# Performance work log

Measured on AMD Instinct MI355X. Metric: run time of the kernel, lower is better.

Reference implementation:

```python
import jax, jax.numpy as jnp
import numpy as np

N = 2_097_152          # n_transitions = n_envs * buffer_size
GAMMA = 0.99
GAE_LAMBDA = 0.95
CLIP_EPS = 0.2
NORM_ADVANTAGES = True


def setup_inputs() -> dict:
    key = jax.random.key(0)
    ks = jax.random.split(key, 7)
    f = lambda k: jax.random.normal(k, (N, 1), dtype=jnp.float32)
    return {
        "rewards": f(ks[0]),
        "values": f(ks[1]),
        "next_values": f(ks[2]),
        "log_probs": -jnp.abs(f(ks[3])),       # log-probs are <= 0
        "old_log_probs": -jnp.abs(f(ks[4])),
        "terminated": jax.random.randint(ks[5], (N, 1), 0, 2).astype(bool),
        "truncated": jax.random.randint(ks[6], (N, 1), 0, 2).astype(bool),
    }


def reference(rewards, values, next_values, log_probs, old_log_probs,
              terminated, truncated):
    dtype = rewards.dtype
    dones = jnp.logical_or(terminated, truncated)
    not_term = 1.0 - terminated.astype(dtype)          # [N,1]
    not_done = 1.0 - dones.astype(dtype)               # [N,1]

    # TD residuals: delta_n = r_n + gamma * (1 - terminated_n) * V(s'_n) - V(s_n)
    deltas = rewards + GAMMA * not_term * next_values - values   # [N,1]

    # Reverse GAE recurrence (the torch Python for-loop, fused into one scan):
    # adv_n = (1 - done_n) * gamma * lambda * adv_{n+1} + delta_n
    coef = not_done[:, 0] * (GAMMA * GAE_LAMBDA)       # [N]

    def step(adv, cd):
        c, d = cd
        adv = c * adv + d
        return adv, adv

    _, advantages = jax.lax.scan(step, jnp.zeros((), dtype),
                                 (coef, deltas[:, 0]), reverse=True)
    advantages = advantages[:, None]                   # [N,1]

    lambda_returns = advantages + values               # [N,1]

    if NORM_ADVANTAGES:
        # torch .std() is the unbiased (ddof=1) estimator
        adv_n = (advantages - advantages.mean()) / (
            jnp.std(advantages, ddof=1) + 1e-9)
    else:
        adv_n = advantages

    # PPO clipped surrogate, per-sample (the .mean() is a trivial reduction)
    ratio = jnp.exp(log_probs - old_log_probs)
    clamped = jnp.clip(ratio, 1.0 - CLIP_EPS, 1.0 + CLIP_EPS)
    per_sample_actor_loss = -jnp.minimum(ratio * adv_n, clamped * adv_n)

    # [N,3]: normalized advantages, lambda returns, per-sample clipped objective
    return jnp.concatenate([adv_n, lambda_returns, per_sample_actor_loss], axis=1)
```

## Files before the change

### kernel.cpp

```cpp
#include <hip/hip_runtime.h>
#include <stdint.h>

static constexpr int BLOCK = 256;
static constexpr int ITEMS = 16;
static constexpr int CHUNK = BLOCK * ITEMS;
static constexpr int MAXNB = 512;

#define GAMMA_F 0.99f
static __device__ __forceinline__ float gl_const() { return (float)(0.99 * 0.95); }

__device__ __forceinline__ int detect_mode(const void* term, int n_elems, int* flg) {
    int t = threadIdx.x;
    if (t == 0) { flg[0] = 0; flg[1] = 0; }
    __syncthreads();
    if (t < 256) {
        const unsigned char* p = (const unsigned char*)term;
        int i0 = 4 * t;
        if (i0 + 3 < n_elems) {
            unsigned b1 = p[i0 + 1], b2 = p[i0 + 2], b3 = p[i0 + 3];
            if (b1) atomicOr(&flg[0], 1);
            if (b2 | b3) atomicOr(&flg[1], 1);
        }
    }
    __syncthreads();
    return flg[0] ? 1 : (flg[1] ? 2 : 0);
}

__device__ __forceinline__ int load_bool1(const void* p, long i, int mode) {
    if (mode == 1) return ((const unsigned char*)p)[i] != 0;
    if (mode == 0) return ((const int*)p)[i] != 0;
    return ((const float*)p)[i] != 0.0f;
}

__device__ __forceinline__ void load_bool16(const void* p, long base, int mode, int* f) {
    if (mode == 1) {
        uint4 q = *(const uint4*)((const unsigned char*)p + base);
        unsigned w[4] = {q.x, q.y, q.z, q.w};
#pragma unroll
        for (int j = 0; j < 16; ++j) f[j] = (int)((w[j >> 2] >> ((j & 3) * 8)) & 0xffu);
    } else if (mode == 0) {
        const int4* q = (const int4*)((const int*)p + base);
#pragma unroll
        for (int k = 0; k < 4; ++k) {
            int4 v = q[k];
            f[4*k] = v.x; f[4*k+1] = v.y; f[4*k+2] = v.z; f[4*k+3] = v.w;
        }
    } else {
        const float4* q = (const float4*)((const float*)p + base);
#pragma unroll
        for (int k = 0; k < 4; ++k) {
            float4 v = q[k];
            f[4*k] = v.x != 0.f; f[4*k+1] = v.y != 0.f; f[4*k+2] = v.z != 0.f; f[4*k+3] = v.w != 0.f;
        }
    }
}

__device__ __forceinline__ void compute_cd(
    const float* __restrict__ rewards, const float* __restrict__ values,
    const float* __restrict__ next_values, const void* __restrict__ term,
    const void* __restrict__ trunc, int mode, long base, int n,
    float* c, float* d, float* v)
{
    const float GL = gl_const();
    if (base + ITEMS <= n) {
        float r[ITEMS], nv[ITEMS];
        const float4* r4 = (const float4*)(rewards + base);
        const float4* v4 = (const float4*)(values + base);
        const float4* n4 = (const float4*)(next_values + base);
#pragma unroll
        for (int k = 0; k < 4; ++k) {
            float4 a = r4[k]; r[4*k]=a.x; r[4*k+1]=a.y; r[4*k+2]=a.z; r[4*k+3]=a.w;
            float4 b = v4[k]; v[4*k]=b.x; v[4*k+1]=b.y; v[4*k+2]=b.z; v[4*k+3]=b.w;
            float4 q = n4[k]; nv[4*k]=q.x; nv[4*k+1]=q.y; nv[4*k+2]=q.z; nv[4*k+3]=q.w;
        }
        int tm[ITEMS], tr[ITEMS];
        load_bool16(term,  base, mode, tm);
        load_bool16(trunc, base, mode, tr);
#pragma unroll
        for (int j = 0; j < ITEMS; ++j) {
            float nt = tm[j] ? 0.f : 1.f;
            float nd = (tm[j] | tr[j]) ? 0.f : 1.f;
            d[j] = r[j] + GAMMA_F * nt * nv[j] - v[j];
            c[j] = nd * GL;
        }
    } else {
#pragma unroll
        for (int j = 0; j < ITEMS; ++j) {
            long i = base + j;
            if (i < (long)n) {
                int tm = load_bool1(term, i, mode);
                int tr = load_bool1(trunc, i, mode);
                float nt = tm ? 0.f : 1.f;
                float nd = (tm | tr) ? 0.f : 1.f;
                v[j] = values[i];
                d[j] = rewards[i] + GAMMA_F * nt * next_values[i] - v[j];
                c[j] = nd * GL;
            } else { c[j] = 1.f; d[j] = 0.f; v[j] = 0.f; }
        }
    }
}

__global__ __launch_bounds__(BLOCK) void k1_agg(
    const float* __restrict__ rewards, const float* __restrict__ values,
    const float* __restrict__ next_values, const void* __restrict__ term,
    const void* __restrict__ trunc, float2* __restrict__ blockAgg, int n)
{
    __shared__ int flg[2];
    __shared__ float sA[BLOCK], sB[BLOCK];
    int mode = detect_mode(term, n, flg);
    int t = threadIdx.x;
    long base = (long)blockIdx.x * CHUNK + (long)t * ITEMS;
    float c[ITEMS], d[ITEMS], v[ITEMS];
    compute_cd(rewards, values, next_values, term, trunc, mode, base, n, c, d, v);
    float a = 1.f, b = 0.f;
#pragma unroll
    for (int j = ITEMS - 1; j >= 0; --j) { b = c[j]*b + d[j]; a = c[j]*a; }
    sA[t] = a; sB[t] = b;
    __syncthreads();
    for (int dd = 1; dd < BLOCK; dd <<= 1) {
        float ra = 1.f, rb = 0.f;
        if (t + dd < BLOCK) { ra = sA[t + dd]; rb = sB[t + dd]; }
        __syncthreads();
        b = a * rb + b;
        a = a * ra;
        sA[t] = a; sB[t] = b;
        __syncthreads();
    }
    if (t == 0) blockAgg[blockIdx.x] = make_float2(a, b);
}

__global__ __launch_bounds__(MAXNB) void k2_scan(
    const float2* __restrict__ blockAgg, float* __restrict__ S,
    double* __restrict__ sums, int nb)
{
    __shared__ float sA[MAXNB], sB[MAXNB];
    int t = threadIdx.x;
    float a = 1.f, b = 0.f;
    if (t < nb) { float2 f = blockAgg[t]; a = f.x; b = f.y; }
    sA[t] = a; sB[t] = b;
    __syncthreads();
    for (int dd = 1; dd < MAXNB; dd <<= 1) {
        float ra = 1.f, rb = 0.f;
        if (t + dd < MAXNB) { ra = sA[t + dd]; rb = sB[t + dd]; }
        __syncthreads();
        b = a * rb + b;
        a = a * ra;
        sA[t] = a; sB[t] = b;
        __syncthreads();
    }
    if (t < nb) S[t] = (t + 1 < nb) ? sB[t + 1] : 0.f;
    if (t == 0) { sums[0] = 0.0; sums[1] = 0.0; }
}

__global__ __launch_bounds__(BLOCK) void k3_adv(
    const float* __restrict__ rewards, const float* __restrict__ values,
    const float* __restrict__ next_values, const void* __restrict__ term,
    const void* __restrict__ trunc, const float* __restrict__ S,
    float* __restrict__ out, double* __restrict__ sums, int n)
{
    __shared__ int flg[2];
    __shared__ float sA[BLOCK], sB[BLOCK];
    int mode = detect_mode(term, n, flg);
    int t = threadIdx.x;
    long base = (long)blockIdx.x * CHUNK + (long)t * ITEMS;
    float c[ITEMS], d[ITEMS], v[ITEMS];
    compute_cd(rewards, values, next_values, term, trunc, mode, base, n, c, d, v);
    float a = 1.f, b = 0.f;
#pragma unroll
    for (int j = ITEMS - 1; j >= 0; --j) { b = c[j]*b + d[j]; a = c[j]*a; }
    sA[t] = a; sB[t] = b;
    __syncthreads();
    for (int dd = 1; dd < BLOCK; dd <<= 1) {
        float ra = 1.f, rb = 0.f;
        if (t + dd < BLOCK) { ra = sA[t + dd]; rb = sB[t + dd]; }
        __syncthreads();
        b = a * rb + b;
        a = a * ra;
        sA[t] = a; sB[t] = b;
        __syncthreads();
    }
    float ea = 1.f, eb = 0.f;
    if (t + 1 < BLOCK) { ea = sA[t + 1]; eb = sB[t + 1]; }
    float x = ea * S[blockIdx.x] + eb;
    float s = 0.f, s2 = 0.f;
    float adv[ITEMS];
#pragma unroll
    for (int j = ITEMS - 1; j >= 0; --j) {
        x = c[j] * x + d[j];
        adv[j] = x;
        if (base + j < (long)n) { s += x; s2 += x * x; }
    }
    if (base + ITEMS <= n) {
#pragma unroll
        for (int j = 0; j < ITEMS; ++j) {
            long o = 3 * (base + j);
            out[o]     = adv[j];
            out[o + 1] = adv[j] + v[j];
        }
    } else {
        for (int j = 0; j < ITEMS; ++j) {
            long i = base + j;
            if (i < (long)n) { long o = 3*i; out[o] = adv[j]; out[o+1] = adv[j] + v[j]; }
        }
    }
    __syncthreads();
    sA[t] = s; sB[t] = s2;
    __syncthreads();
    for (int dd = BLOCK / 2; dd > 0; dd >>= 1) {
        if (t < dd) { sA[t] += sA[t + dd]; sB[t] += sB[t + dd]; }
        __syncthreads();
    }
    if (t == 0) {
        atomicAdd(&sums[0], (double)sA[0]);
        atomicAdd(&sums[1], (double)sB[0]);
    }
}

__global__ __launch_bounds__(BLOCK) void k4_final(
    const float* __restrict__ lp, const float* __restrict__ olp,
    const double* __restrict__ sums, float* __restrict__ out, int n)
{
    long e = ((long)blockIdx.x * blockDim.x + threadIdx.x) * 4;
    if (e >= n) return;
    double sum = sums[0], sumsq = sums[1];
    float mean = (float)(sum / (double)n);
    double var = (sumsq - sum * sum / (double)n) / (double)(n - 1);
    if (var < 0.0) var = 0.0;
    float inv = 1.0f / ((float)sqrt(var) + 1e-9f);
    if (e + 4 <= n) {
        float4 l  = *(const float4*)(lp + e);
        float4 o  = *(const float4*)(olp + e);
        float4 t0 = *(float4*)(out + 3 * e);
        float4 t1 = *(float4*)(out + 3 * e + 4);
        float4 t2 = *(float4*)(out + 3 * e + 8);
        float advv[4] = {t0.x, t0.w, t1.z, t2.y};
        float lv[4]   = {l.x, l.y, l.z, l.w};
        float ov[4]   = {o.x, o.y, o.z, o.w};
        float an[4], ls[4];
#pragma unroll
        for (int j = 0; j < 4; ++j) {
            an[j] = (advv[j] - mean) * inv;
            float ratio = expf(lv[j] - ov[j]);
            float cl = fminf(fmaxf(ratio, 0.8f), 1.2f);
            ls[j] = -fminf(ratio * an[j], cl * an[j]);
        }
        t0.x = an[0]; t0.z = ls[0]; t0.w = an[1];
        t1.y = ls[1]; t1.z = an[2];
        t2.x = ls[2]; t2.y = an[3]; t2.w = ls[3];
        *(float4*)(out + 3 * e)     = t0;
        *(float4*)(out + 3 * e + 4) = t1;
        *(float4*)(out + 3 * e + 8) = t2;
    } else {
        for (long i = e; i < (long)n; ++i) {
            float advv = out[3 * i];
            float an = (advv - mean) * inv;
            float ratio = expf(lp[i] - olp[i]);
            float cl = fminf(fmaxf(ratio, 0.8f), 1.2f);
            out[3 * i]     = an;
            out[3 * i + 2] = -fminf(ratio * an, cl * an);
        }
    }
}

extern "C" void kernel_launch(void* const* d_in, const int* in_sizes, int n_in,
                              void* d_out, int out_size, void* d_ws, size_t ws_size,
                              hipStream_t stream) {
    const float* rewards     = (const float*)d_in[0];
    const float* values      = (const float*)d_in[1];
    const float* next_values = (const float*)d_in[2];
    const float* lp          = (const float*)d_in[3];
    const float* olp         = (const float*)d_in[4];
    const void*  term        = d_in[5];
    const void*  trunc       = d_in[6];
    float* out = (float*)d_out;
    int n = in_sizes[0];

    double* sums     = (double*)d_ws;
    float2* blockAgg = (float2*)((char*)d_ws + 64);
    float*  S        = (float*)((char*)d_ws + 64 + MAXNB * sizeof(float2));

    int nb = (n + CHUNK - 1) / CHUNK;

    k1_agg <<<nb, BLOCK, 0, stream>>>(rewards, values, next_values, term, trunc, blockAgg, n);
    k2_scan<<<1, MAXNB, 0, stream>>>(blockAgg, S, sums, nb);
    k3_adv <<<nb, BLOCK, 0, stream>>>(rewards, values, next_values, term, trunc, S, out, sums, n);
    int n4blocks = (int)(((long)n / 4 + BLOCK - 1) / BLOCK);
    k4_final<<<n4blocks, BLOCK, 0, stream>>>(lp, olp, sums, out, n);
}
```

Before: 154.9 us.

## Fuse four-kernel GAE/PPO pipeline into one cooperative kernel with grid syncs

Replaces the four kernels (block aggregate, block-prefix scan, advantage pass, final normalize/loss pass) with a single cooperative kernel that uses grid.sync between phases. Each block keeps its loaded c/d/v and computed advantages in registers, so the inputs are read once instead of twice and the output is written once as full float4 rows rather than written partially then read back and rewritten. Block sums are reduced deterministically in double by block 0 instead of through double atomics. The cost is four grid-wide barriers, a serial single-block phase, and the requirement that all 512 blocks be co-resident for the cooperative launch.

After: 350.9 us. 2.26x slower.

```diff
diff --git a/kernel.cpp b/kernel.cpp
--- a/kernel.cpp
+++ b/kernel.cpp
@@ -1,5 +1,8 @@
 #include <hip/hip_runtime.h>
+#include <hip/hip_cooperative_groups.h>
 #include <stdint.h>
+
+namespace cg = cooperative_groups;
 
 static constexpr int BLOCK = 256;
 static constexpr int ITEMS = 16;
@@ -100,18 +103,28 @@
     }
 }
 
-__global__ __launch_bounds__(BLOCK) void k1_agg(
+__global__ __launch_bounds__(BLOCK, 2) void ppo_fused(
     const float* __restrict__ rewards, const float* __restrict__ values,
-    const float* __restrict__ next_values, const void* __restrict__ term,
-    const void* __restrict__ trunc, float2* __restrict__ blockAgg, int n)
+    const float* __restrict__ next_values, const float* __restrict__ lp,
+    const float* __restrict__ olp, const void* __restrict__ term,
+    const void* __restrict__ trunc, float* __restrict__ out,
+    float2* __restrict__ blockAgg, float* __restrict__ S,
+    float2* __restrict__ blockSums, float* __restrict__ stats,
+    int n, int nb)
 {
     __shared__ int flg[2];
     __shared__ float sA[BLOCK], sB[BLOCK];
-    int mode = detect_mode(term, n, flg);
-    int t = threadIdx.x;
-    long base = (long)blockIdx.x * CHUNK + (long)t * ITEMS;
+    __shared__ double dS[BLOCK], dS2[BLOCK];
+    cg::grid_group grid = cg::this_grid();
+
+    const int t = threadIdx.x;
+    const int bid = blockIdx.x;
+    const int mode = detect_mode(term, n, flg);
+    const long base = (long)bid * CHUNK + (long)t * ITEMS;
+
     float c[ITEMS], d[ITEMS], v[ITEMS];
     compute_cd(rewards, values, next_values, term, trunc, mode, base, n, c, d, v);
+
     float a = 1.f, b = 0.f;
 #pragma unroll
     for (int j = ITEMS - 1; j >= 0; --j) { b = c[j]*b + d[j]; a = c[j]*a; }
@@ -126,138 +139,114 @@
         sA[t] = a; sB[t] = b;
         __syncthreads();
     }
-    if (t == 0) blockAgg[blockIdx.x] = make_float2(a, b);
-}
-
-__global__ __launch_bounds__(MAXNB) void k2_scan(
-    const float2* __restrict__ blockAgg, float* __restrict__ S,
-    double* __restrict__ sums, int nb)
-{
-    __shared__ float sA[MAXNB], sB[MAXNB];
-    int t = threadIdx.x;
-    float a = 1.f, b = 0.f;
-    if (t < nb) { float2 f = blockAgg[t]; a = f.x; b = f.y; }
-    sA[t] = a; sB[t] = b;
-    __syncthreads();
-    for (int dd = 1; dd < MAXNB; dd <<= 1) {
-        float ra = 1.f, rb = 0.f;
-        if (t + dd < MAXNB) { ra = sA[t + dd]; rb = sB[t + dd]; }
-        __syncthreads();
-        b = a * rb + b;
-        a = a * ra;
-        sA[t] = a; sB[t] = b;
-        __syncthreads();
-    }
-    if (t < nb) S[t] = (t + 1 < nb) ? sB[t + 1] : 0.f;
-    if (t == 0) { sums[0] = 0.0; sums[1] = 0.0; }
-}
-
-__global__ __launch_bounds__(BLOCK) void k3_adv(
-    const float* __restrict__ rewards, const float* __restrict__ values,
-    const float* __restrict__ next_values, const void* __restrict__ term,
-    const void* __restrict__ trunc, const float* __restrict__ S,
-    float* __restrict__ out, double* __restrict__ sums, int n)
-{
-    __shared__ int flg[2];
-    __shared__ float sA[BLOCK], sB[BLOCK];
-    int mode = detect_mode(term, n, flg);
-    int t = threadIdx.x;
-    long base = (long)blockIdx.x * CHUNK + (long)t * ITEMS;
-    float c[ITEMS], d[ITEMS], v[ITEMS];
-    compute_cd(rewards, values, next_values, term, trunc, mode, base, n, c, d, v);
-    float a = 1.f, b = 0.f;
-#pragma unroll
-    for (int j = ITEMS - 1; j >= 0; --j) { b = c[j]*b + d[j]; a = c[j]*a; }
-    sA[t] = a; sB[t] = b;
-    __syncthreads();
-    for (int dd = 1; dd < BLOCK; dd <<= 1) {
-        float ra = 1.f, rb = 0.f;
-        if (t + dd < BLOCK) { ra = sA[t + dd]; rb = sB[t + dd]; }
-        __syncthreads();
-        b = a * rb + b;
-        a = a * ra;
-        sA[t] = a; sB[t] = b;
-        __syncthreads();
-    }
     float ea = 1.f, eb = 0.f;
     if (t + 1 < BLOCK) { ea = sA[t + 1]; eb = sB[t + 1]; }
-    float x = ea * S[blockIdx.x] + eb;
+    if (t == 0) blockAgg[bid] = make_float2(a, b);
+
+    grid.sync();
+
+    if (bid == 0) {
+        const int i0 = 2 * t, i1 = 2 * t + 1;
+        float a0 = 1.f, b0 = 0.f, a1 = 1.f, b1 = 0.f;
+        if (i0 < nb) { float2 f = blockAgg[i0]; a0 = f.x; b0 = f.y; }
+        if (i1 < nb) { float2 f = blockAgg[i1]; a1 = f.x; b1 = f.y; }
+        float fa = a0 * a1, fb = a0 * b1 + b0;
+        float pa = fa, pb = fb;
+        sA[t] = pa; sB[t] = pb;
+        __syncthreads();
+        for (int dd = 1; dd < BLOCK; dd <<= 1) {
+            float ra = 1.f, rb = 0.f;
+            if (t + dd < BLOCK) { ra = sA[t + dd]; rb = sB[t + dd]; }
+            __syncthreads();
+            pb = pa * rb + pb;
+            pa = pa * ra;
+            sA[t] = pa; sB[t] = pb;
+            __syncthreads();
+        }
+        float Eb = 0.f;
+        if (t + 1 < BLOCK) { Eb = sB[t + 1]; }
+        if (i1 < nb) S[i1] = Eb;
+        if (i0 < nb) S[i0] = a1 * Eb + b1;
+    }
+
+    grid.sync();
+
+    float x = ea * S[bid] + eb;
+    float adv[ITEMS];
     float s = 0.f, s2 = 0.f;
-    float adv[ITEMS];
 #pragma unroll
     for (int j = ITEMS - 1; j >= 0; --j) {
         x = c[j] * x + d[j];
         adv[j] = x;
         if (base + j < (long)n) { s += x; s2 += x * x; }
     }
-    if (base + ITEMS <= n) {
-#pragma unroll
-        for (int j = 0; j < ITEMS; ++j) {
-            long o = 3 * (base + j);
-            out[o]     = adv[j];
-            out[o + 1] = adv[j] + v[j];
-        }
-    } else {
-        for (int j = 0; j < ITEMS; ++j) {
-            long i = base + j;
-            if (i < (long)n) { long o = 3*i; out[o] = adv[j]; out[o+1] = adv[j] + v[j]; }
-        }
-    }
-    __syncthreads();
     sA[t] = s; sB[t] = s2;
     __syncthreads();
     for (int dd = BLOCK / 2; dd > 0; dd >>= 1) {
         if (t < dd) { sA[t] += sA[t + dd]; sB[t] += sB[t + dd]; }
         __syncthreads();
     }
-    if (t == 0) {
-        atomicAdd(&sums[0], (double)sA[0]);
-        atomicAdd(&sums[1], (double)sB[0]);
-    }
-}
-
-__global__ __launch_bounds__(BLOCK) void k4_final(
-    const float* __restrict__ lp, const float* __restrict__ olp,
-    const double* __restrict__ sums, float* __restrict__ out, int n)
-{
-    long e = ((long)blockIdx.x * blockDim.x + threadIdx.x) * 4;
-    if (e >= n) return;
-    double sum = sums[0], sumsq = sums[1];
-    float mean = (float)(sum / (double)n);
-    double var = (sumsq - sum * sum / (double)n) / (double)(n - 1);
-    if (var < 0.0) var = 0.0;
-    float inv = 1.0f / ((float)sqrt(var) + 1e-9f);
-    if (e + 4 <= n) {
-        float4 l  = *(const float4*)(lp + e);
-        float4 o  = *(const float4*)(olp + e);
-        float4 t0 = *(float4*)(out + 3 * e);
-        float4 t1 = *(float4*)(out + 3 * e + 4);
-        float4 t2 = *(float4*)(out + 3 * e + 8);
-        float advv[4] = {t0.x, t0.w, t1.z, t2.y};
-        float lv[4]   = {l.x, l.y, l.z, l.w};
-        float ov[4]   = {o.x, o.y, o.z, o.w};
-        float an[4], ls[4];
-#pragma unroll
-        for (int j = 0; j < 4; ++j) {
-            an[j] = (advv[j] - mean) * inv;
-            float ratio = expf(lv[j] - ov[j]);
+    if (t == 0) blockSums[bid] = make_float2(sA[0], sB[0]);
+
+    grid.sync();
+
+    if (bid == 0) {
+        double ds = 0.0, ds2 = 0.0;
+        for (int i = t; i < nb; i += BLOCK) { float2 f = blockSums[i]; ds += (double)f.x; ds2 += (double)f.y; }
+        dS[t] = ds; dS2[t] = ds2;
+        __syncthreads();
+        for (int dd = BLOCK / 2; dd > 0; dd >>= 1) {
+            if (t < dd) { dS[t] += dS[t + dd]; dS2[t] += dS2[t + dd]; }
+            __syncthreads();
+        }
+        if (t == 0) {
+            double sum = dS[0], sumsq = dS2[0];
+            double mean = sum / (double)n;
+            double var = (sumsq - sum * sum / (double)n) / (double)(n - 1);
+            if (var < 0.0) var = 0.0;
+            stats[0] = (float)mean;
+            stats[1] = 1.0f / ((float)sqrt(var) + 1e-9f);
+        }
+    }
+
+    grid.sync();
+
+    const float mean = stats[0];
+    const float inv  = stats[1];
+    if (base + ITEMS <= n) {
+        float l[ITEMS], o[ITEMS];
+        const float4* l4 = (const float4*)(lp + base);
+        const float4* o4 = (const float4*)(olp + base);
+#pragma unroll
+        for (int k = 0; k < 4; ++k) {
+            float4 q = l4[k]; l[4*k]=q.x; l[4*k+1]=q.y; l[4*k+2]=q.z; l[4*k+3]=q.w;
+            float4 w = o4[k]; o[4*k]=w.x; o[4*k+1]=w.y; o[4*k+2]=w.z; o[4*k+3]=w.w;
+        }
+        float buf[3 * ITEMS];
+#pragma unroll
+        for (int j = 0; j < ITEMS; ++j) {
+            float an = (adv[j] - mean) * inv;
+            float ratio = expf(l[j] - o[j]);
             float cl = fminf(fmaxf(ratio, 0.8f), 1.2f);
-            ls[j] = -fminf(ratio * an[j], cl * an[j]);
-        }
-        t0.x = an[0]; t0.z = ls[0]; t0.w = an[1];
-        t1.y = ls[1]; t1.z = an[2];
-        t2.x = ls[2]; t2.y = an[3]; t2.w = ls[3];
-        *(float4*)(out + 3 * e)     = t0;
-        *(float4*)(out + 3 * e + 4) = t1;
-        *(float4*)(out + 3 * e + 8) = t2;
+            buf[3*j]     = an;
+            buf[3*j + 1] = adv[j] + v[j];
+            buf[3*j + 2] = -fminf(ratio * an, cl * an);
+        }
+        float4* dst = (float4*)(out + 3 * base);
+#pragma unroll
+        for (int k = 0; k < 12; ++k)
+            dst[k] = make_float4(buf[4*k], buf[4*k+1], buf[4*k+2], buf[4*k+3]);
     } else {
-        for (long i = e; i < (long)n; ++i) {
-            float advv = out[3 * i];
-            float an = (advv - mean) * inv;
-            float ratio = expf(lp[i] - olp[i]);
-            float cl = fminf(fmaxf(ratio, 0.8f), 1.2f);
-            out[3 * i]     = an;
-            out[3 * i + 2] = -fminf(ratio * an, cl * an);
+        for (int j = 0; j < ITEMS; ++j) {
+            long i = base + j;
+            if (i < (long)n) {
+                float an = (adv[j] - mean) * inv;
+                float ratio = expf(lp[i] - olp[i]);
+                float cl = fminf(fmaxf(ratio, 0.8f), 1.2f);
+                out[3*i]     = an;
+                out[3*i + 1] = adv[j] + v[j];
+                out[3*i + 2] = -fminf(ratio * an, cl * an);
+            }
         }
     }
 }
@@ -274,16 +263,16 @@
     const void*  trunc       = d_in[6];
     float* out = (float*)d_out;
     int n = in_sizes[0];
-
-    double* sums     = (double*)d_ws;
-    float2* blockAgg = (float2*)((char*)d_ws + 64);
-    float*  S        = (float*)((char*)d_ws + 64 + MAXNB * sizeof(float2));
-
     int nb = (n + CHUNK - 1) / CHUNK;
 
-    k1_agg <<<nb, BLOCK, 0, stream>>>(rewards, values, next_values, term, trunc, blockAgg, n);
-    k2_scan<<<1, MAXNB, 0, stream>>>(blockAgg, S, sums, nb);
-    k3_adv <<<nb, BLOCK, 0, stream>>>(rewards, values, next_values, term, trunc, S, out, sums, n);
-    int n4blocks = (int)(((long)n / 4 + BLOCK - 1) / BLOCK);
-    k4_final<<<n4blocks, BLOCK, 0, stream>>>(lp, olp, sums, out, n);
-}
+    char* ws = (char*)d_ws;
+    float2* blockAgg  = (float2*)ws;
+    float*  S         = (float*) (ws + MAXNB * 8);
+    float2* blockSums = (float2*)(ws + MAXNB * 8 + MAXNB * 4);
+    float*  stats     = (float*) (ws + MAXNB * 8 + MAXNB * 4 + MAXNB * 8);
+
+    void* args[] = { &rewards, &values, &next_values, &lp, &olp, &term, &trunc,
+                     &out, &blockAgg, &S, &blockSums, &stats, &n, &nb };
+    hipLaunchCooperativeKernel((void*)ppo_fused, dim3(nb), dim3(BLOCK),
+                               args, 0, stream);
+}
```

## Stage advantages in contiguous workspace, drop atomics, write interleaved output once

Applied to the files above, without the earlier changes.

k3_adv now writes the advantages to a contiguous workspace array with vector stores, where it used to do strided scalar writes into the interleaved output. Its per-block sums go to a buffer that a new single-block kernel reduces in double. That kernel also computes mean and inverse std once, replacing the double atomics. k4_final reads advs, values, lp and olp contiguously and writes all three output columns in one pass of full float4 stores, avoiding a read-modify-write of the output. ITEMS drops to 8 (twice as many blocks), and k2_scan handles up to 1024 block aggregates with 256 threads doing 4 each; the cost is an extra kernel launch and a re-read of values.

After: 136.1 us. 1.14x faster.

```diff
diff --git a/kernel.cpp b/kernel.cpp
--- a/kernel.cpp
+++ b/kernel.cpp
@@ -2,9 +2,9 @@
 #include <stdint.h>
 
 static constexpr int BLOCK = 256;
-static constexpr int ITEMS = 16;
+static constexpr int ITEMS = 8;
 static constexpr int CHUNK = BLOCK * ITEMS;
-static constexpr int MAXNB = 512;
+static constexpr int MAXNB = 1024;
 
 #define GAMMA_F 0.99f
 static __device__ __forceinline__ float gl_const() { return (float)(0.99 * 0.95); }
@@ -32,23 +32,23 @@
     return ((const float*)p)[i] != 0.0f;
 }
 
-__device__ __forceinline__ void load_bool16(const void* p, long base, int mode, int* f) {
+__device__ __forceinline__ void load_bool8(const void* p, long base, int mode, int* f) {
     if (mode == 1) {
-        uint4 q = *(const uint4*)((const unsigned char*)p + base);
-        unsigned w[4] = {q.x, q.y, q.z, q.w};
-#pragma unroll
-        for (int j = 0; j < 16; ++j) f[j] = (int)((w[j >> 2] >> ((j & 3) * 8)) & 0xffu);
+        uint2 q = *(const uint2*)((const unsigned char*)p + base);
+        unsigned w[2] = {q.x, q.y};
+#pragma unroll
+        for (int j = 0; j < 8; ++j) f[j] = (int)((w[j >> 2] >> ((j & 3) * 8)) & 0xffu);
     } else if (mode == 0) {
         const int4* q = (const int4*)((const int*)p + base);
 #pragma unroll
-        for (int k = 0; k < 4; ++k) {
+        for (int k = 0; k < 2; ++k) {
             int4 v = q[k];
             f[4*k] = v.x; f[4*k+1] = v.y; f[4*k+2] = v.z; f[4*k+3] = v.w;
         }
     } else {
         const float4* q = (const float4*)((const float*)p + base);
 #pragma unroll
-        for (int k = 0; k < 4; ++k) {
+        for (int k = 0; k < 2; ++k) {
             float4 v = q[k];
             f[4*k] = v.x != 0.f; f[4*k+1] = v.y != 0.f; f[4*k+2] = v.z != 0.f; f[4*k+3] = v.w != 0.f;
         }
@@ -68,14 +68,14 @@
         const float4* v4 = (const float4*)(values + base);
         const float4* n4 = (const float4*)(next_values + base);
 #pragma unroll
-        for (int k = 0; k < 4; ++k) {
+        for (int k = 0; k < 2; ++k) {
             float4 a = r4[k]; r[4*k]=a.x; r[4*k+1]=a.y; r[4*k+2]=a.z; r[4*k+3]=a.w;
             float4 b = v4[k]; v[4*k]=b.x; v[4*k+1]=b.y; v[4*k+2]=b.z; v[4*k+3]=b.w;
             float4 q = n4[k]; nv[4*k]=q.x; nv[4*k+1]=q.y; nv[4*k+2]=q.z; nv[4*k+3]=q.w;
         }
         int tm[ITEMS], tr[ITEMS];
-        load_bool16(term,  base, mode, tm);
-        load_bool16(trunc, base, mode, tr);
+        load_bool8(term,  base, mode, tm);
+        load_bool8(trunc, base, mode, tr);
 #pragma unroll
         for (int j = 0; j < ITEMS; ++j) {
             float nt = tm[j] ? 0.f : 1.f;
@@ -129,34 +129,47 @@
     if (t == 0) blockAgg[blockIdx.x] = make_float2(a, b);
 }
 
-__global__ __launch_bounds__(MAXNB) void k2_scan(
-    const float2* __restrict__ blockAgg, float* __restrict__ S,
-    double* __restrict__ sums, int nb)
-{
-    __shared__ float sA[MAXNB], sB[MAXNB];
-    int t = threadIdx.x;
+__global__ __launch_bounds__(BLOCK) void k2_scan(
+    const float2* __restrict__ blockAgg, float* __restrict__ S, int nb)
+{
+    __shared__ float sA[BLOCK], sB[BLOCK];
+    const int t = threadIdx.x;
+    float la[4], lb[4];
+#pragma unroll
+    for (int j = 0; j < 4; ++j) {
+        int i = 4 * t + j;
+        if (i < nb) { float2 f = blockAgg[i]; la[j] = f.x; lb[j] = f.y; }
+        else        { la[j] = 1.f; lb[j] = 0.f; }
+    }
     float a = 1.f, b = 0.f;
-    if (t < nb) { float2 f = blockAgg[t]; a = f.x; b = f.y; }
+#pragma unroll
+    for (int j = 3; j >= 0; --j) { b = la[j] * b + lb[j]; a = la[j] * a; }
     sA[t] = a; sB[t] = b;
     __syncthreads();
-    for (int dd = 1; dd < MAXNB; dd <<= 1) {
+    for (int dd = 1; dd < BLOCK; dd <<= 1) {
         float ra = 1.f, rb = 0.f;
-        if (t + dd < MAXNB) { ra = sA[t + dd]; rb = sB[t + dd]; }
+        if (t + dd < BLOCK) { ra = sA[t + dd]; rb = sB[t + dd]; }
         __syncthreads();
         b = a * rb + b;
         a = a * ra;
         sA[t] = a; sB[t] = b;
         __syncthreads();
     }
-    if (t < nb) S[t] = (t + 1 < nb) ? sB[t + 1] : 0.f;
-    if (t == 0) { sums[0] = 0.0; sums[1] = 0.0; }
+    float x = (t + 1 < BLOCK) ? sB[t + 1] : 0.f;
+    if (4 * t + 3 < nb) S[4 * t + 3] = x;
+    x = la[3] * x + lb[3];
+    if (4 * t + 2 < nb) S[4 * t + 2] = x;
+    x = la[2] * x + lb[2];
+    if (4 * t + 1 < nb) S[4 * t + 1] = x;
+    x = la[1] * x + lb[1];
+    if (4 * t     < nb) S[4 * t    ] = x;
 }
 
 __global__ __launch_bounds__(BLOCK) void k3_adv(
     const float* __restrict__ rewards, const float* __restrict__ values,
     const float* __restrict__ next_values, const void* __restrict__ term,
     const void* __restrict__ trunc, const float* __restrict__ S,
-    float* __restrict__ out, double* __restrict__ sums, int n)
+    float* __restrict__ advs, float2* __restrict__ blockSums, int n)
 {
     __shared__ int flg[2];
     __shared__ float sA[BLOCK], sB[BLOCK];
@@ -182,8 +195,8 @@
     float ea = 1.f, eb = 0.f;
     if (t + 1 < BLOCK) { ea = sA[t + 1]; eb = sB[t + 1]; }
     float x = ea * S[blockIdx.x] + eb;
+    float adv[ITEMS];
     float s = 0.f, s2 = 0.f;
-    float adv[ITEMS];
 #pragma unroll
     for (int j = ITEMS - 1; j >= 0; --j) {
         x = c[j] * x + d[j];
@@ -191,17 +204,12 @@
         if (base + j < (long)n) { s += x; s2 += x * x; }
     }
     if (base + ITEMS <= n) {
-#pragma unroll
-        for (int j = 0; j < ITEMS; ++j) {
-            long o = 3 * (base + j);
-            out[o]     = adv[j];
-            out[o + 1] = adv[j] + v[j];
-        }
+        float4* dst = (float4*)(advs + base);
+        dst[0] = make_float4(adv[0], adv[1], adv[2], adv[3]);
+        dst[1] = make_float4(adv[4], adv[5], adv[6], adv[7]);
     } else {
-        for (int j = 0; j < ITEMS; ++j) {
-            long i = base + j;
-            if (i < (long)n) { long o = 3*i; out[o] = adv[j]; out[o+1] = adv[j] + v[j]; }
-        }
+        for (int j = 0; j < ITEMS; ++j)
+            if (base + j < (long)n) advs[base + j] = adv[j];
     }
     __syncthreads();
     sA[t] = s; sB[t] = s2;
@@ -210,54 +218,76 @@
         if (t < dd) { sA[t] += sA[t + dd]; sB[t] += sB[t + dd]; }
         __syncthreads();
     }
+    if (t == 0) blockSums[blockIdx.x] = make_float2(sA[0], sB[0]);
+}
+
+__global__ __launch_bounds__(BLOCK) void k3b_stats(
+    const float2* __restrict__ blockSums, float* __restrict__ stats, int nb, int n)
+{
+    __shared__ double dS[BLOCK], dS2[BLOCK];
+    const int t = threadIdx.x;
+    double s = 0.0, s2 = 0.0;
+    for (int i = t; i < nb; i += BLOCK) {
+        float2 f = blockSums[i];
+        s += (double)f.x; s2 += (double)f.y;
+    }
+    dS[t] = s; dS2[t] = s2;
+    __syncthreads();
+    for (int dd = BLOCK / 2; dd > 0; dd >>= 1) {
+        if (t < dd) { dS[t] += dS[t + dd]; dS2[t] += dS2[t + dd]; }
+        __syncthreads();
+    }
     if (t == 0) {
-        atomicAdd(&sums[0], (double)sA[0]);
-        atomicAdd(&sums[1], (double)sB[0]);
+        double sum = dS[0], sumsq = dS2[0];
+        double mean = sum / (double)n;
+        double var = (sumsq - sum * sum / (double)n) / (double)(n - 1);
+        if (var < 0.0) var = 0.0;
+        stats[0] = (float)mean;
+        stats[1] = 1.0f / ((float)sqrt(var) + 1e-9f);
     }
 }
 
 __global__ __launch_bounds__(BLOCK) void k4_final(
+    const float* __restrict__ advs, const float* __restrict__ values,
     const float* __restrict__ lp, const float* __restrict__ olp,
-    const double* __restrict__ sums, float* __restrict__ out, int n)
+    const float* __restrict__ stats, float* __restrict__ out, int n)
 {
     long e = ((long)blockIdx.x * blockDim.x + threadIdx.x) * 4;
     if (e >= n) return;
-    double sum = sums[0], sumsq = sums[1];
-    float mean = (float)(sum / (double)n);
-    double var = (sumsq - sum * sum / (double)n) / (double)(n - 1);
-    if (var < 0.0) var = 0.0;
-    float inv = 1.0f / ((float)sqrt(var) + 1e-9f);
+    const float mean = stats[0];
+    const float inv  = stats[1];
     if (e + 4 <= n) {
-        float4 l  = *(const float4*)(lp + e);
-        float4 o  = *(const float4*)(olp + e);
-        float4 t0 = *(float4*)(out + 3 * e);
-        float4 t1 = *(float4*)(out + 3 * e + 4);
-        float4 t2 = *(float4*)(out + 3 * e + 8);
-        float advv[4] = {t0.x, t0.w, t1.z, t2.y};
-        float lv[4]   = {l.x, l.y, l.z, l.w};
-        float ov[4]   = {o.x, o.y, o.z, o.w};
-        float an[4], ls[4];
+        float4 a4 = *(const float4*)(advs + e);
+        float4 v4 = *(const float4*)(values + e);
+        float4 l4 = *(const float4*)(lp + e);
+        float4 o4 = *(const float4*)(olp + e);
+        float av[4] = {a4.x, a4.y, a4.z, a4.w};
+        float vv[4] = {v4.x, v4.y, v4.z, v4.w};
+        float lv[4] = {l4.x, l4.y, l4.z, l4.w};
+        float ov[4] = {o4.x, o4.y, o4.z, o4.w};
+        float buf[12];
 #pragma unroll
         for (int j = 0; j < 4; ++j) {
-            an[j] = (advv[j] - mean) * inv;
+            float an = (av[j] - mean) * inv;
             float ratio = expf(lv[j] - ov[j]);
             float cl = fminf(fmaxf(ratio, 0.8f), 1.2f);
-            ls[j] = -fminf(ratio * an[j], cl * an[j]);
-        }
-        t0.x = an[0]; t0.z = ls[0]; t0.w = an[1];
-        t1.y = ls[1]; t1.z = an[2];
-        t2.x = ls[2]; t2.y = an[3]; t2.w = ls[3];
-        *(float4*)(out + 3 * e)     = t0;
-        *(float4*)(out + 3 * e + 4) = t1;
-        *(float4*)(out + 3 * e + 8) = t2;
+            buf[3*j]     = an;
+            buf[3*j + 1] = av[j] + vv[j];
+            buf[3*j + 2] = -fminf(ratio * an, cl * an);
+        }
+        float4* dst = (float4*)(out + 3 * e);
+        dst[0] = make_float4(buf[0], buf[1], buf[2],  buf[3]);
+        dst[1] = make_float4(buf[4], buf[5], buf[6],  buf[7]);
+        dst[2] = make_float4(buf[8], buf[9], buf[10], buf[11]);
     } else {
         for (long i = e; i < (long)n; ++i) {
-            float advv = out[3 * i];
-            float an = (advv - mean) * inv;
+            float a = advs[i];
+            float an = (a - mean) * inv;
             float ratio = expf(lp[i] - olp[i]);
             float cl = fminf(fmaxf(ratio, 0.8f), 1.2f);
-            out[3 * i]     = an;
-            out[3 * i + 2] = -fminf(ratio * an, cl * an);
+            out[3*i]     = an;
+            out[3*i + 1] = a + values[i];
+            out[3*i + 2] = -fminf(ratio * an, cl * an);
         }
     }
 }
@@ -274,16 +304,20 @@
     const void*  trunc       = d_in[6];
     float* out = (float*)d_out;
     int n = in_sizes[0];
-
-    double* sums     = (double*)d_ws;
-    float2* blockAgg = (float2*)((char*)d_ws + 64);
-    float*  S        = (float*)((char*)d_ws + 64 + MAXNB * sizeof(float2));
-
     int nb = (n + CHUNK - 1) / CHUNK;
 
-    k1_agg <<<nb, BLOCK, 0, stream>>>(rewards, values, next_values, term, trunc, blockAgg, n);
-    k2_scan<<<1, MAXNB, 0, stream>>>(blockAgg, S, sums, nb);
-    k3_adv <<<nb, BLOCK, 0, stream>>>(rewards, values, next_values, term, trunc, S, out, sums, n);
+    char* ws = (char*)d_ws;
+    size_t advs_bytes = (((size_t)n * 4) + 255) & ~(size_t)255;
+    float*  advs      = (float*)ws;
+    float2* blockAgg  = (float2*)(ws + advs_bytes);
+    float*  S         = (float*)(ws + advs_bytes + MAXNB * 8);
+    float2* blockSums = (float2*)(ws + advs_bytes + MAXNB * 8 + MAXNB * 4);
+    float*  stats     = (float*)(ws + advs_bytes + MAXNB * 8 + MAXNB * 4 + MAXNB * 8);
+
+    k1_agg   <<<nb, BLOCK, 0, stream>>>(rewards, values, next_values, term, trunc, blockAgg, n);
+    k2_scan  <<<1,  BLOCK, 0, stream>>>(blockAgg, S, nb);
+    k3_adv   <<<nb, BLOCK, 0, stream>>>(rewards, values, next_values, term, trunc, S, advs, blockSums, n);
+    k3b_stats<<<1,  BLOCK, 0, stream>>>(blockSums, stats, nb, n);
     int n4blocks = (int)(((long)n / 4 + BLOCK - 1) / BLOCK);
-    k4_final<<<n4blocks, BLOCK, 0, stream>>>(lp, olp, sums, out, n);
-}
+    k4_final <<<n4blocks, BLOCK, 0, stream>>>(advs, values, lp, olp, stats, out, n);
+}
```
